# Optimization experiments

Measured on AMD Instinct MI355X. Metric: run time of the kernel, lower is better.

Reference implementation:

```python
import jax, jax.numpy as jnp
import numpy as np

EPS = 1e-05


def setup_inputs() -> dict:
    key = jax.random.key(0)
    ks = jax.random.split(key, 6)
    B, L, D = 16, 4096, 1024
    x = jax.random.normal(ks[0], (B, L, D), dtype=jnp.float32)
    prev_count = jax.random.randint(ks[1], (B,), 1, 5).astype(jnp.int32)  # prior_count-like, >=1
    prev_mean = jnp.zeros((B, D), dtype=jnp.float32)   # prior_mean init = 0
    prev_var = jnp.ones((B, D), dtype=jnp.float32)     # exp(prior_logv) with logv init 0
    weight = 0.02 * jax.random.normal(ks[2], (D,), dtype=jnp.float32)
    bias = 0.02 * jax.random.normal(ks[3], (D,), dtype=jnp.float32)
    padding_mask = jax.random.randint(ks[4], (B, L), 0, 2).astype(bool)  # True = padded
    return {"x": x, "prev_count": prev_count, "prev_mean": prev_mean,
            "prev_var": prev_var, "weight": weight, "bias": bias,
            "padding_mask": padding_mask}


def _timestep_norm(x, prev_count, prev_mean, prev_var, gamma, beta, padding_mask, eps):
    # x: [B, L, D]; Welford running mean/var over timesteps, skipping padded steps.
    B, L, D = x.shape
    valid = (~padding_mask).astype(x.dtype)          # [B, L], 1 = valid step
    x_t = jnp.swapaxes(x, 0, 1)                      # [L, B, D]
    m_t = valid.T                                    # [L, B]

    def step(carry, inp):
        count, mean, var = carry                     # [B], [B,D], [B,D]
        xt, m = inp                                  # [B,D], [B]
        mb = m[:, None]                              # [B,1]
        new_count = count + m                        # [B]
        denom = jnp.maximum(new_count, 1.0)[:, None]
        delta = xt - mean
        new_mean = mean + mb * delta / denom
        var_upd = (count[:, None] * var + delta * (xt - new_mean)) / denom
        new_var = jnp.where(mb > 0, var_upd, var)
        y = (gamma * (xt - new_mean) * jax.lax.rsqrt(new_var + eps) + beta) * mb
        return (new_count, new_mean, new_var), y

    init = (prev_count.astype(x.dtype), prev_mean, prev_var)
    (count, mean, var), ys = jax.lax.scan(step, init, (x_t, m_t))
    y = jnp.swapaxes(ys, 0, 1)                       # [B, L, D]
    return y, count, mean, var


def reference(x, prev_count, prev_mean, prev_var, weight, bias, padding_mask):
    gamma = weight + 1.0
    return _timestep_norm(x, prev_count, prev_mean, prev_var, gamma, bias,
                          padding_mask, EPS)
```

## Files before the change

kernel.cpp:

```cpp
#include <hip/hip_runtime.h>


#define Bn 16
#define Ln 4096
#define Dn 1024
#define D4 (Dn / 4)
#define Cn 128
#define CLn (Ln / Cn)
#define NCH (Bn * Cn)
#define EPSf 1e-5f

typedef float f32x4 __attribute__((ext_vector_type(4)));

struct St { float n; float4 m; float4 s; };

__device__ __forceinline__ St chan_merge(const St& A, const St& B) {
    St R;
    R.n = A.n + B.n;
    float wB = B.n / fmaxf(R.n, 1.f);
    float sc = A.n * wB;
    float dx = B.m.x - A.m.x, dy = B.m.y - A.m.y,
          dz = B.m.z - A.m.z, dw = B.m.w - A.m.w;
    R.m.x = A.m.x + dx * wB; R.m.y = A.m.y + dy * wB;
    R.m.z = A.m.z + dz * wB; R.m.w = A.m.w + dw * wB;
    R.s.x = A.s.x + B.s.x + dx * dx * sc; R.s.y = A.s.y + B.s.y + dy * dy * sc;
    R.s.z = A.s.z + B.s.z + dz * dz * sc; R.s.w = A.s.w + B.s.w + dw * dw * sc;
    return R;
}

__device__ __forceinline__ St shfl_up_st(const St& v, int delta) {
    St r;
    r.n   = __shfl_up(v.n,   delta, 64);
    r.m.x = __shfl_up(v.m.x, delta, 64); r.m.y = __shfl_up(v.m.y, delta, 64);
    r.m.z = __shfl_up(v.m.z, delta, 64); r.m.w = __shfl_up(v.m.w, delta, 64);
    r.s.x = __shfl_up(v.s.x, delta, 64); r.s.y = __shfl_up(v.s.y, delta, 64);
    r.s.z = __shfl_up(v.s.z, delta, 64); r.s.w = __shfl_up(v.s.w, delta, 64);
    return r;
}

__global__ __launch_bounds__(256) void tn_chunk_stats(
    const float* __restrict__ x, const int* __restrict__ mask,
    float4* __restrict__ agg_mean, float4* __restrict__ agg_m2,
    float* __restrict__ agg_n)
{
    int bc = blockIdx.x;
    int d4 = threadIdx.x;
    const float4* xp = (const float4*)(x + (size_t)bc * CLn * Dn) + d4;
    const int4*   mp = (const int4*)(mask + bc * CLn);

    int4 mrow[CLn / 4];
    #pragma unroll
    for (int i = 0; i < CLn / 4; ++i) mrow[i] = mp[i];
    const int* mr = (const int*)mrow;

    St A; A.n = 0.f; A.m = {0.f, 0.f, 0.f, 0.f}; A.s = {0.f, 0.f, 0.f, 0.f};
    #pragma unroll 8
    for (int i = 0; i < CLn; ++i) {
        if (mr[i] == 0) {
            float4 xv = xp[(size_t)i * D4];
            A.n += 1.f;
            float rn = 1.f / A.n;
            float dx;
            dx = xv.x - A.m.x; A.m.x += dx * rn; A.s.x += dx * (xv.x - A.m.x);
            dx = xv.y - A.m.y; A.m.y += dx * rn; A.s.y += dx * (xv.y - A.m.y);
            dx = xv.z - A.m.z; A.m.z += dx * rn; A.s.z += dx * (xv.z - A.m.z);
            dx = xv.w - A.m.w; A.m.w += dx * rn; A.s.w += dx * (xv.w - A.m.w);
        }
    }
    agg_mean[(size_t)bc * D4 + d4] = A.m;
    agg_m2  [(size_t)bc * D4 + d4] = A.s;
    if (d4 == 0) agg_n[bc] = A.n;
}

__global__ __launch_bounds__(256) void tn_scan(
    const int* __restrict__ prev_count, const float4* __restrict__ prev_mean,
    const float4* __restrict__ prev_var,
    const float4* __restrict__ agg_mean, const float4* __restrict__ agg_m2,
    const float* __restrict__ agg_n,
    float4* __restrict__ pref_mean, float4* __restrict__ pref_m2,
    float* __restrict__ pref_n,
    float* __restrict__ out_count, float4* __restrict__ out_mean,
    float4* __restrict__ out_var)
{
    int wv   = (blockIdx.x * 256 + threadIdx.x) >> 6;
    int lane = threadIdx.x & 63;
    int b  = wv >> 8;
    int d4 = wv & (D4 - 1);
    int c0 = 2 * lane, c1 = 2 * lane + 1;
    int ch0 = b * Cn + c0, ch1 = b * Cn + c1;

    St s0, s1;
    s0.n = agg_n[ch0]; s0.m = agg_mean[(size_t)ch0 * D4 + d4]; s0.s = agg_m2[(size_t)ch0 * D4 + d4];
    s1.n = agg_n[ch1]; s1.m = agg_mean[(size_t)ch1 * D4 + d4]; s1.s = agg_m2[(size_t)ch1 * D4 + d4];

    St incl = chan_merge(s0, s1);
    #pragma unroll
    for (int off = 1; off < 64; off <<= 1) {
        St t = shfl_up_st(incl, off);
        if (lane >= off) incl = chan_merge(t, incl);
    }
    St epp = shfl_up_st(incl, 1);
    if (lane == 0) {
        epp.n = 0.f;
        epp.m = {0.f, 0.f, 0.f, 0.f};
        epp.s = {0.f, 0.f, 0.f, 0.f};
    }

    float np = (float)prev_count[b];
    St P;
    P.n = np;
    P.m = prev_mean[b * D4 + d4];
    float4 vp = prev_var[b * D4 + d4];
    P.s = {vp.x * np, vp.y * np, vp.z * np, vp.w * np};

    St pref0 = chan_merge(P, epp);
    St pref1 = chan_merge(pref0, s0);

    pref_mean[(size_t)ch0 * D4 + d4] = pref0.m; pref_m2[(size_t)ch0 * D4 + d4] = pref0.s;
    pref_mean[(size_t)ch1 * D4 + d4] = pref1.m; pref_m2[(size_t)ch1 * D4 + d4] = pref1.s;
    if (d4 == 0) {
        pref_n[ch0] = pref0.n;
        pref_n[ch1] = pref1.n;
    }

    if (lane == 63) {
        St tot = chan_merge(P, incl);
        out_mean[b * D4 + d4] = tot.m;
        float rn = 1.f / tot.n;
        out_var[b * D4 + d4] = {tot.s.x * rn, tot.s.y * rn, tot.s.z * rn, tot.s.w * rn};
        if (d4 == 0) out_count[b] = tot.n;
    }
}

__global__ __launch_bounds__(256) void tn_emit(
    const float* __restrict__ x, const int* __restrict__ mask,
    const float* __restrict__ weight, const float* __restrict__ bias,
    const float4* __restrict__ pref_mean, const float4* __restrict__ pref_m2,
    const float* __restrict__ pref_n, float* __restrict__ y)
{
    int bc = blockIdx.x;
    int d4 = threadIdx.x;
    size_t gbase = (size_t)bc * CLn * Dn;
    const float4* xp = (const float4*)(x + gbase) + d4;
    f32x4*        yp = (f32x4*)(y + gbase) + d4;
    const int4*   mp = (const int4*)(mask + bc * CLn);

    int4 mrow[CLn / 4];
    #pragma unroll
    for (int i = 0; i < CLn / 4; ++i) mrow[i] = mp[i];
    const int* mr = (const int*)mrow;

    float  n    = pref_n[bc];
    float4 mean = pref_mean[(size_t)bc * D4 + d4];
    float4 M2   = pref_m2  [(size_t)bc * D4 + d4];
    const float4 w4 = ((const float4*)weight)[d4];
    const float4 b4 = ((const float4*)bias)[d4];
    float gx = w4.x + 1.f, gy = w4.y + 1.f, gz = w4.z + 1.f, gw = w4.w + 1.f;

    #pragma unroll 4
    for (int i = 0; i < CLn; ++i) {
        f32x4 yv = {0.f, 0.f, 0.f, 0.f};
        if (mr[i] == 0) {
            float4 xv = xp[(size_t)i * D4];
            n += 1.f;
            float rn = 1.f / n;
            float dx, d2;
            dx = xv.x - mean.x; mean.x += dx * rn; d2 = xv.x - mean.x;
            M2.x += dx * d2; yv.x = gx * d2 * rsqrtf(M2.x * rn + EPSf) + b4.x;
            dx = xv.y - mean.y; mean.y += dx * rn; d2 = xv.y - mean.y;
            M2.y += dx * d2; yv.y = gy * d2 * rsqrtf(M2.y * rn + EPSf) + b4.y;
            dx = xv.z - mean.z; mean.z += dx * rn; d2 = xv.z - mean.z;
            M2.z += dx * d2; yv.z = gz * d2 * rsqrtf(M2.z * rn + EPSf) + b4.z;
            dx = xv.w - mean.w; mean.w += dx * rn; d2 = xv.w - mean.w;
            M2.w += dx * d2; yv.w = gw * d2 * rsqrtf(M2.w * rn + EPSf) + b4.w;
        }
        __builtin_nontemporal_store(yv, &yp[(size_t)i * D4]);
    }
}

extern "C" void kernel_launch(void* const* d_in, const int* in_sizes, int n_in,
                              void* d_out, int out_size, void* d_ws, size_t ws_size,
                              hipStream_t stream)
{
    const float* x          = (const float*)d_in[0];
    const int*   prev_count = (const int*)d_in[1];
    const float* prev_mean  = (const float*)d_in[2];
    const float* prev_var   = (const float*)d_in[3];
    const float* weight     = (const float*)d_in[4];
    const float* bias       = (const float*)d_in[5];
    const int*   mask       = (const int*)d_in[6];

    float* y         = (float*)d_out;
    float* out_count = y + (size_t)Bn * Ln * Dn;
    float* out_mean  = out_count + Bn;
    float* out_var   = out_mean + (size_t)Bn * Dn;

    float4* agg_mean  = (float4*)d_ws;
    float4* agg_m2    = agg_mean  + (size_t)NCH * D4;
    float4* pref_mean = agg_m2    + (size_t)NCH * D4;
    float4* pref_m2   = pref_mean + (size_t)NCH * D4;
    float*  agg_n     = (float*)(pref_m2 + (size_t)NCH * D4);
    float*  pref_n    = agg_n + NCH;

    tn_chunk_stats<<<NCH, 256, 0, stream>>>(x, mask, agg_mean, agg_m2, agg_n);
    tn_scan<<<(Bn * D4) / 4, 256, 0, stream>>>(
        prev_count, (const float4*)prev_mean, (const float4*)prev_var,
        agg_mean, agg_m2, agg_n, pref_mean, pref_m2, pref_n,
        out_count, (float4*)out_mean, (float4*)out_var);
    tn_emit<<<NCH, 256, 0, stream>>>(
        x, mask, weight, bias, pref_mean, pref_m2, pref_n, y);
}
```

Baseline: 502.1 us.

## Halve chunk count, stage mask in LDS, use nontemporal x loads in emit

Reduces the number of timestep chunks per batch from 128 to 64, so each chunk spans 64 steps. The scan now maps one chunk per lane instead of two, which removes the pairwise pre-merge. Both streaming kernels load the padding mask into shared memory instead of per-thread register arrays, and the emit kernel reads x with nontemporal loads. With only 1024 blocks per streaming kernel and longer serial chains per thread, latency hiding may drop, while workspace traffic and scan work shrink.

```diff
diff --git a/kernel.cpp b/kernel.cpp
--- a/kernel.cpp
+++ b/kernel.cpp
@@ -5,7 +5,7 @@
 #define Ln 4096
 #define Dn 1024
 #define D4 (Dn / 4)
-#define Cn 128
+#define Cn 64
 #define CLn (Ln / Cn)
 #define NCH (Bn * Cn)
 #define EPSf 1e-5f
@@ -45,18 +45,16 @@
 {
     int bc = blockIdx.x;
     int d4 = threadIdx.x;
+    __shared__ int smask[CLn];
+    if (threadIdx.x < CLn) smask[threadIdx.x] = mask[bc * CLn + threadIdx.x];
+    __syncthreads();
+
     const float4* xp = (const float4*)(x + (size_t)bc * CLn * Dn) + d4;
-    const int4*   mp = (const int4*)(mask + bc * CLn);
-
-    int4 mrow[CLn / 4];
-    #pragma unroll
-    for (int i = 0; i < CLn / 4; ++i) mrow[i] = mp[i];
-    const int* mr = (const int*)mrow;
 
     St A; A.n = 0.f; A.m = {0.f, 0.f, 0.f, 0.f}; A.s = {0.f, 0.f, 0.f, 0.f};
-    #pragma unroll 8
+    #pragma unroll 4
     for (int i = 0; i < CLn; ++i) {
-        if (mr[i] == 0) {
+        if (smask[i] == 0) {
             float4 xv = xp[(size_t)i * D4];
             A.n += 1.f;
             float rn = 1.f / A.n;
@@ -86,24 +84,24 @@
     int lane = threadIdx.x & 63;
     int b  = wv >> 8;
     int d4 = wv & (D4 - 1);
-    int c0 = 2 * lane, c1 = 2 * lane + 1;
-    int ch0 = b * Cn + c0, ch1 = b * Cn + c1;
-
-    St s0, s1;
-    s0.n = agg_n[ch0]; s0.m = agg_mean[(size_t)ch0 * D4 + d4]; s0.s = agg_m2[(size_t)ch0 * D4 + d4];
-    s1.n = agg_n[ch1]; s1.m = agg_mean[(size_t)ch1 * D4 + d4]; s1.s = agg_m2[(size_t)ch1 * D4 + d4];
-
-    St incl = chan_merge(s0, s1);
+    int ch = b * Cn + lane;
+
+    St s0;
+    s0.n = agg_n[ch];
+    s0.m = agg_mean[(size_t)ch * D4 + d4];
+    s0.s = agg_m2  [(size_t)ch * D4 + d4];
+
+    St incl = s0;
     #pragma unroll
     for (int off = 1; off < 64; off <<= 1) {
         St t = shfl_up_st(incl, off);
         if (lane >= off) incl = chan_merge(t, incl);
     }
-    St epp = shfl_up_st(incl, 1);
+    St excl = shfl_up_st(incl, 1);
     if (lane == 0) {
-        epp.n = 0.f;
-        epp.m = {0.f, 0.f, 0.f, 0.f};
-        epp.s = {0.f, 0.f, 0.f, 0.f};
+        excl.n = 0.f;
+        excl.m = {0.f, 0.f, 0.f, 0.f};
+        excl.s = {0.f, 0.f, 0.f, 0.f};
     }
 
     float np = (float)prev_count[b];
@@ -113,15 +111,11 @@
     float4 vp = prev_var[b * D4 + d4];
     P.s = {vp.x * np, vp.y * np, vp.z * np, vp.w * np};
 
-    St pref0 = chan_merge(P, epp);
-    St pref1 = chan_merge(pref0, s0);
-
-    pref_mean[(size_t)ch0 * D4 + d4] = pref0.m; pref_m2[(size_t)ch0 * D4 + d4] = pref0.s;
-    pref_mean[(size_t)ch1 * D4 + d4] = pref1.m; pref_m2[(size_t)ch1 * D4 + d4] = pref1.s;
-    if (d4 == 0) {
-        pref_n[ch0] = pref0.n;
-        pref_n[ch1] = pref1.n;
-    }
+    St pref = chan_merge(P, excl);
+
+    pref_mean[(size_t)ch * D4 + d4] = pref.m;
+    pref_m2  [(size_t)ch * D4 + d4] = pref.s;
+    if (d4 == 0) pref_n[ch] = pref.n;
 
     if (lane == 63) {
         St tot = chan_merge(P, incl);
@@ -140,15 +134,13 @@
 {
     int bc = blockIdx.x;
     int d4 = threadIdx.x;
+    __shared__ int smask[CLn];
+    if (threadIdx.x < CLn) smask[threadIdx.x] = mask[bc * CLn + threadIdx.x];
+    __syncthreads();
+
     size_t gbase = (size_t)bc * CLn * Dn;
-    const float4* xp = (const float4*)(x + gbase) + d4;
-    f32x4*        yp = (f32x4*)(y + gbase) + d4;
-    const int4*   mp = (const int4*)(mask + bc * CLn);
-
-    int4 mrow[CLn / 4];
-    #pragma unroll
-    for (int i = 0; i < CLn / 4; ++i) mrow[i] = mp[i];
-    const int* mr = (const int*)mrow;
+    const f32x4* xp = (const f32x4*)(x + gbase) + d4;
+    f32x4*       yp = (f32x4*)(y + gbase) + d4;
 
     float  n    = pref_n[bc];
     float4 mean = pref_mean[(size_t)bc * D4 + d4];
@@ -160,8 +152,8 @@
     #pragma unroll 4
     for (int i = 0; i < CLn; ++i) {
         f32x4 yv = {0.f, 0.f, 0.f, 0.f};
-        if (mr[i] == 0) {
-            float4 xv = xp[(size_t)i * D4];
+        if (smask[i] == 0) {
+            f32x4 xv = __builtin_nontemporal_load(&xp[(size_t)i * D4]);
             n += 1.f;
             float rn = 1.f / n;
             float dx, d2;
@@ -203,7 +195,7 @@
     float*  pref_n    = agg_n + NCH;
 
     tn_chunk_stats<<<NCH, 256, 0, stream>>>(x, mask, agg_mean, agg_m2, agg_n);
-    tn_scan<<<(Bn * D4) / 4, 256, 0, stream>>>(
+    tn_scan<<<(Bn * D4 * 64) / 256, 256, 0, stream>>>(
         prev_count, (const float4*)prev_mean, (const float4*)prev_var,
         agg_mean, agg_m2, agg_n, pref_mean, pref_m2, pref_n,
         out_count, (float4*)out_mean, (float4*)out_var);
```

After: 447.7 us. -10.8%, faster.
